# Optimization experiments

Measured on AMD Instinct MI355X. Metric: run time of the kernel, lower is better.

The kernel has to match this reference:

```python
import jax, jax.numpy as jnp
import numpy as np

N, C, L, K = 8, 128, 1024, 100   # batch, channels, encoded seq len, num_negatives
TEMP = 0.5                        # contrastive temperature
EPS = 1e-8                        # cosine-similarity norm clamp (torch default)


def setup_inputs() -> dict:
    key = jax.random.key(0)
    kz, kc, kn = jax.random.split(key, 3)
    z = jax.random.normal(kz, (N, C, L), dtype=jnp.float32)
    c = jax.random.normal(kc, (N, C, L + 1), dtype=jnp.float32)
    # Uniform sampling of K distinct indices per (n, l), excluding l itself:
    # equivalent to torch.multinomial(ones(L,L)-eye(L), K) per row, per sample.
    noise = jax.random.uniform(kn, (N, L, L), dtype=jnp.float32)
    noise = noise - 2.0 * jnp.eye(L, dtype=jnp.float32)  # push self-index below everything
    _, neg_inds = jax.lax.top_k(noise, K)                # (N, L, K) int32, distinct, != l
    return {"z": z, "c": c, "neg_inds": neg_inds.astype(jnp.int32)}


def reference(z, c, neg_inds):
    # z: (N, C, L) unmasked convencoder features; c: (N, C, L+1) transformer out
    n, ch, l = z.shape
    z_seq = jnp.transpose(z, (0, 2, 1))                  # (N, L, C)
    # gather negatives: (N, L, K, C)
    negatives = z_seq[jnp.arange(n)[:, None, None], neg_inds]
    # drop start token, move to (N, L, 1, C)
    c_seq = jnp.transpose(c[..., 1:], (0, 2, 1))[:, :, None, :]
    z_tgt = z_seq[:, :, None, :]                         # (N, L, 1, C)
    targets = jnp.concatenate([z_tgt, negatives], axis=2)  # (N, L, K+1, C)
    # cosine similarity along C with torch-style eps clamping
    dot = jnp.sum(c_seq * targets, axis=-1)              # (N, L, K+1)
    c_norm = jnp.maximum(jnp.sqrt(jnp.sum(c_seq * c_seq, axis=-1)), EPS)
    t_norm = jnp.maximum(jnp.sqrt(jnp.sum(targets * targets, axis=-1)), EPS)
    logits = dot / (c_norm * t_norm) / TEMP              # (N, L, K+1)
    # mask negatives that exactly equal the context vector
    neg_in_tgt = jnp.all(c_seq == negatives, axis=-1)    # (N, L, K)
    neg_logits = jnp.where(neg_in_tgt, -jnp.inf, logits[:, :, 1:])
    logits = jnp.concatenate([logits[:, :, :1], neg_logits], axis=2)
    return logits.reshape(-1, K + 1)                     # (N*L, K+1)
```

## Files before the change

kernel.cpp:

```cpp
#include <hip/hip_runtime.h>
#include <math.h>

#define N 8
#define C 128
#define L 1024
#define K 100
#define TEMP 0.5f
#define EPS 1e-8f
#define NT (N * L)
#define ROWS 16

typedef _Float16 half8 __attribute__((ext_vector_type(8)));
typedef float f32x4 __attribute__((ext_vector_type(4)));

__global__ void __launch_bounds__(512)
transpose_both(const float* __restrict__ z, const float* __restrict__ c,
               _Float16* __restrict__ z_h, _Float16* __restrict__ c_h,
               float* __restrict__ zp, float* __restrict__ cp) {
    __shared__ float tile[64][65];
    __shared__ float part[8][64];
    const int which = blockIdx.z >> 3;
    const int n = blockIdx.z & 7;
    const float* src = which ? c : z;
    _Float16* dst = which ? c_h : z_h;
    float* pdst = which ? cp : zp;
    const int slen = which ? (L + 1) : L;
    const int off = which;
    const int l0 = blockIdx.x * 64;
    const int c0 = blockIdx.y * 64;
    const int tx = threadIdx.x;
    const int ty = threadIdx.y;
#pragma unroll
    for (int i = 0; i < 8; i++) {
        int chn = c0 + ty + i * 8;
        tile[ty + i * 8][tx] = src[((size_t)(n * C + chn)) * slen + off + l0 + tx];
    }
    __syncthreads();
#pragma unroll
    for (int i = 0; i < 8; i++) {
        int l = l0 + ty + i * 8;
        dst[((size_t)n * L + l) * C + c0 + tx] = (_Float16)tile[tx][ty + i * 8];
    }
    float p = 0.f;
#pragma unroll
    for (int i = 0; i < 8; i++) { float v = tile[ty * 8 + i][tx]; p += v * v; }
    part[ty][tx] = p;
    __syncthreads();
    if (ty == 0) {
        float sm = 0.f;
#pragma unroll
        for (int i = 0; i < 8; i++) sm += part[i][tx];
        pdst[(((size_t)n << 10) + l0 + tx) * 2 + (c0 >> 6)] = sm;
    }
}

__global__ void __launch_bounds__(512)
gemm_gather(const _Float16* __restrict__ zh, const _Float16* __restrict__ ch,
            const int* __restrict__ neg_inds,
            const float* __restrict__ zp, const float* __restrict__ cp,
            const float* __restrict__ z_orig, const float* __restrict__ c_orig,
            float* __restrict__ out) {
    __shared__ float dotL[ROWS * L];
    const int tid  = threadIdx.x;
    const int lane = tid & 63;
    const int w    = tid >> 6;
    const int n    = blockIdx.x >> 6;
    const int t0   = (blockIdx.x & 63) * ROWS;

    const int r16 = lane & 15;
    const int kg  = lane >> 4;

    const _Float16* Abase = ch + ((size_t)(n * L + t0)) * C;
    const _Float16* Bbase = zh + ((size_t)(n * L)) * C;

    half8 a[4];
#pragma unroll
    for (int ks = 0; ks < 4; ks++)
        a[ks] = *(const half8*)(Abase + (size_t)r16 * C + ks * 32 + kg * 8);

    f32x4 acc[8];
#pragma unroll
    for (int i = 0; i < 8; i++)
#pragma unroll
        for (int r = 0; r < 4; r++) acc[i][r] = 0.f;

    const int c0w = w << 7;
#pragma unroll
    for (int ks = 0; ks < 4; ks++) {
#pragma unroll
        for (int nt = 0; nt < 8; nt++) {
            const half8 b = *(const half8*)(Bbase
                + (size_t)(c0w + nt * 16 + r16) * C + ks * 32 + kg * 8);
            acc[nt] = __builtin_amdgcn_mfma_f32_16x16x32_f16(a[ks], b, acc[nt], 0, 0, 0);
        }
    }

#pragma unroll
    for (int nt = 0; nt < 8; nt++)
#pragma unroll
        for (int r = 0; r < 4; r++)
            dotL[(kg * 4 + r) * L + c0w + nt * 16 + r16] = acc[nt][r];

    __syncthreads();

    const int row = tid >> 5;
    const int sub = tid & 31;
    const int t   = t0 + row;
    const int ntg = (n << 10) + t;
    const float2 cpv = ((const float2*)cp)[ntg];
    const float cn = cpv.x + cpv.y;
    const float rs_c = 2.0f * rsqrtf(fmaxf(cn, EPS * EPS));
    const int* ni = neg_inds + (size_t)ntg * K;
    const float2* zp2 = (const float2*)zp + ((size_t)n << 10);
    float* orow = out + (size_t)ntg * (K + 1);

    for (int kk = sub; kk <= K; kk += 32) {
        const int col = (kk == 0) ? t : ni[kk - 1];
        const float dot = dotL[row * L + col];
        const float2 tv = zp2[col];
        const float tn = tv.x + tv.y;
        float logit = dot * rs_c * rsqrtf(fmaxf(tn, EPS * EPS));
        if (kk > 0) {
            const float ds = cn - 2.f * dot + tn;
            if (ds < 0.05f * cn) {
                bool eq = true;
                for (int q = 0; q < C; q++) {
                    float cv = c_orig[((size_t)(n * C + q)) * (L + 1) + t + 1];
                    float zv = z_orig[((size_t)(n * C + q)) * L + col];
                    eq = eq && (cv == zv);
                }
                if (eq) logit = -INFINITY;
            }
        }
        orow[kk] = logit;
    }
}

extern "C" void kernel_launch(void* const* d_in, const int* in_sizes, int n_in,
                              void* d_out, int out_size, void* d_ws, size_t ws_size,
                              hipStream_t stream) {
    const float* z   = (const float*)d_in[0];
    const float* c   = (const float*)d_in[1];
    const int*   neg = (const int*)d_in[2];
    float* out = (float*)d_out;

    _Float16* z_h = (_Float16*)d_ws;
    _Float16* c_h = z_h + (size_t)NT * C;
    float* zp = (float*)(c_h + (size_t)NT * C);
    float* cp = zp + (size_t)NT * 2;

    transpose_both<<<dim3(L / 64, C / 64, 16), dim3(64, 8), 0, stream>>>(z, c, z_h, c_h, zp, cp);
    gemm_gather<<<dim3(N * (L / ROWS)), 512, 0, stream>>>(z_h, c_h, neg, zp, cp, z, c, out);
}
```

Before: 86.79 us.

## Store fp16 operands in MFMA fragment order and swizzle LDS dot tile

The transpose kernel now writes z and c as half8 vectors already arranged in MFMA fragment order, so each lane in the GEMM loads one contiguous 16-byte fragment instead of strided row reads. The shared-memory dot tile uses an XOR swizzle on the column index to reduce bank conflicts when the accumulators are stored and when the gather reads them. The per-column z norms are also staged into LDS before the gather. Together these add coupling between the producer and consumer layouts and use extra LDS.

Result: faster. 77.14 us (-11.1%).

```diff
diff --git a/kernel.cpp b/kernel.cpp
--- a/kernel.cpp
+++ b/kernel.cpp
@@ -8,21 +8,21 @@
 #define TEMP 0.5f
 #define EPS 1e-8f
 #define NT (N * L)
-#define ROWS 16
 
 typedef _Float16 half8 __attribute__((ext_vector_type(8)));
 typedef float f32x4 __attribute__((ext_vector_type(4)));
 
+
 __global__ void __launch_bounds__(512)
-transpose_both(const float* __restrict__ z, const float* __restrict__ c,
-               _Float16* __restrict__ z_h, _Float16* __restrict__ c_h,
+transpose_frag(const float* __restrict__ z, const float* __restrict__ c,
+               half8* __restrict__ zf, half8* __restrict__ cf,
                float* __restrict__ zp, float* __restrict__ cp) {
     __shared__ float tile[64][65];
     __shared__ float part[8][64];
     const int which = blockIdx.z >> 3;
     const int n = blockIdx.z & 7;
     const float* src = which ? c : z;
-    _Float16* dst = which ? c_h : z_h;
+    half8* dst = which ? cf : zf;
     float* pdst = which ? cp : zp;
     const int slen = which ? (L + 1) : L;
     const int off = which;
@@ -36,14 +36,18 @@
         tile[ty + i * 8][tx] = src[((size_t)(n * C + chn)) * slen + off + l0 + tx];
     }
     __syncthreads();
+    float p = 0.f;
+    half8 hv;
 #pragma unroll
-    for (int i = 0; i < 8; i++) {
-        int l = l0 + ty + i * 8;
-        dst[((size_t)n * L + l) * C + c0 + tx] = (_Float16)tile[tx][ty + i * 8];
+    for (int q = 0; q < 8; q++) {
+        float v = tile[ty * 8 + q][tx];
+        p += v * v;
+        hv[q] = (_Float16)v;
     }
-    float p = 0.f;
-#pragma unroll
-    for (int i = 0; i < 8; i++) { float v = tile[ty * 8 + i][tx]; p += v * v; }
+    const int l = l0 + tx;
+    const int ch = c0 + ty * 8;
+    const int ks = ch >> 5, kg = (ch >> 3) & 3;
+    dst[(((size_t)(n * 64 + (l >> 4)) * 4 + ks) << 6) + (l & 15) + (kg << 4)] = hv;
     part[ty][tx] = p;
     __syncthreads();
     if (ty == 0) {
@@ -55,28 +59,27 @@
 }
 
 __global__ void __launch_bounds__(512)
-gemm_gather(const _Float16* __restrict__ zh, const _Float16* __restrict__ ch,
+gemm_gather(const half8* __restrict__ zf, const half8* __restrict__ cf,
             const int* __restrict__ neg_inds,
             const float* __restrict__ zp, const float* __restrict__ cp,
             const float* __restrict__ z_orig, const float* __restrict__ c_orig,
             float* __restrict__ out) {
-    __shared__ float dotL[ROWS * L];
+    __shared__ float dotL[16 * L];
+    __shared__ float2 zpl[L];
     const int tid  = threadIdx.x;
     const int lane = tid & 63;
     const int w    = tid >> 6;
     const int n    = blockIdx.x >> 6;
-    const int t0   = (blockIdx.x & 63) * ROWS;
+    const int tA   = blockIdx.x & 63;
 
-    const int r16 = lane & 15;
-    const int kg  = lane >> 4;
+    const float2* zp2 = (const float2*)zp + ((size_t)n << 10);
+    for (int i = tid; i < L; i += 512) zpl[i] = zp2[i];
 
-    const _Float16* Abase = ch + ((size_t)(n * L + t0)) * C;
-    const _Float16* Bbase = zh + ((size_t)(n * L)) * C;
-
+    const size_t nbase = (size_t)n << 14;
     half8 a[4];
 #pragma unroll
     for (int ks = 0; ks < 4; ks++)
-        a[ks] = *(const half8*)(Abase + (size_t)r16 * C + ks * 32 + kg * 8);
+        a[ks] = cf[nbase + (((tA << 2) + ks) << 6) + lane];
 
     f32x4 acc[8];
 #pragma unroll
@@ -84,40 +87,41 @@
 #pragma unroll
         for (int r = 0; r < 4; r++) acc[i][r] = 0.f;
 
-    const int c0w = w << 7;
 #pragma unroll
     for (int ks = 0; ks < 4; ks++) {
 #pragma unroll
         for (int nt = 0; nt < 8; nt++) {
-            const half8 b = *(const half8*)(Bbase
-                + (size_t)(c0w + nt * 16 + r16) * C + ks * 32 + kg * 8);
+            const half8 b = zf[nbase + ((size_t)(((w << 3) + nt) * 4 + ks) << 6) + lane];
             acc[nt] = __builtin_amdgcn_mfma_f32_16x16x32_f16(a[ks], b, acc[nt], 0, 0, 0);
         }
     }
 
+    const int r16 = lane & 15;
+    const int kg  = lane >> 4;
 #pragma unroll
     for (int nt = 0; nt < 8; nt++)
 #pragma unroll
-        for (int r = 0; r < 4; r++)
-            dotL[(kg * 4 + r) * L + c0w + nt * 16 + r16] = acc[nt][r];
-
+        for (int r = 0; r < 4; r++) {
+            const int row = (kg << 2) + r;
+            const int col = (((w << 3) + nt) << 4) + r16;
+            dotL[(row << 10) + (col ^ (row << 1))] = acc[nt][r];
+        }
     __syncthreads();
 
     const int row = tid >> 5;
     const int sub = tid & 31;
-    const int t   = t0 + row;
+    const int t   = (tA << 4) + row;
     const int ntg = (n << 10) + t;
     const float2 cpv = ((const float2*)cp)[ntg];
     const float cn = cpv.x + cpv.y;
     const float rs_c = 2.0f * rsqrtf(fmaxf(cn, EPS * EPS));
     const int* ni = neg_inds + (size_t)ntg * K;
-    const float2* zp2 = (const float2*)zp + ((size_t)n << 10);
     float* orow = out + (size_t)ntg * (K + 1);
 
     for (int kk = sub; kk <= K; kk += 32) {
         const int col = (kk == 0) ? t : ni[kk - 1];
-        const float dot = dotL[row * L + col];
-        const float2 tv = zp2[col];
+        const float dot = dotL[(row << 10) + (col ^ (row << 1))];
+        const float2 tv = zpl[col];
         const float tn = tv.x + tv.y;
         float logit = dot * rs_c * rsqrtf(fmaxf(tn, EPS * EPS));
         if (kk > 0) {
@@ -144,11 +148,11 @@
     const int*   neg = (const int*)d_in[2];
     float* out = (float*)d_out;
 
-    _Float16* z_h = (_Float16*)d_ws;
-    _Float16* c_h = z_h + (size_t)NT * C;
-    float* zp = (float*)(c_h + (size_t)NT * C);
+    half8* zf = (half8*)d_ws;
+    half8* cf = zf + (size_t)N * 16384;
+    float* zp = (float*)(cf + (size_t)N * 16384);
     float* cp = zp + (size_t)NT * 2;
 
-    transpose_both<<<dim3(L / 64, C / 64, 16), dim3(64, 8), 0, stream>>>(z, c, z_h, c_h, zp, cp);
-    gemm_gather<<<dim3(N * (L / ROWS)), 512, 0, stream>>>(z_h, c_h, neg, zp, cp, z, c, out);
+    transpose_frag<<<dim3(L / 64, C / 64, 16), dim3(64, 8), 0, stream>>>(z, c, zf, cf, zp, cp);
+    gemm_gather<<<dim3(N * (L / 16)), 512, 0, stream>>>(zf, cf, neg, zp, cp, z, c, out);
 }
```
